# Kernel tuning notes

Hardware: AMD Instinct MI355X
Metric: run time of the kernel (lower is better)

Reference implementation:

```python
import jax, jax.numpy as jnp
import numpy as np

D = 128          # hidden_channels
NU = 50000       # num user nodes
NI = 50000       # num item nodes
E = 600000       # edges per edge type
SLOPE = 0.01     # F.leaky_relu default negative_slope


def setup_inputs() -> dict:
    key = jax.random.key(0)
    ks = jax.random.split(key, 24)
    ws = 1.0 / np.sqrt(D)  # xavier-ish scale

    def W2(i):  # stacked [n_layers=2, D, D] weight
        return jax.random.normal(ks[i], (2, D, D), jnp.float32) * ws

    def B2(i):  # stacked [2, D] bias
        return jax.random.normal(ks[i], (2, D), jnp.float32) * 0.01

    inp = {
        "x_user": jax.random.normal(ks[0], (NU, D), jnp.float32),
        "x_item": jax.random.normal(ks[1], (NI, D), jnp.float32),
        # row 0 = src indices, row 1 = dst indices
        "ei_ui": jax.random.randint(ks[2], (2, E), 0, NU),  # user -> item (dst in [0,NI))
        "ei_iu": jax.random.randint(ks[3], (2, E), 0, NI),  # item -> user (dst in [0,NU))
        # per-node-type q/k/v Linear params, stacked over the 2 layers
        "q_w_user": W2(4),  "q_b_user": B2(5),
        "k_w_user": W2(6),  "k_b_user": B2(7),
        "v_w_user": W2(8),  "v_b_user": B2(9),
        "q_w_item": W2(10), "q_b_item": B2(11),
        "k_w_item": W2(12), "k_b_item": B2(13),
        "v_w_item": W2(14), "v_b_item": B2(15),
        # per-edge-type bilinear W, stacked over the 2 layers
        "W_ui": W2(16),
        "W_iu": W2(17),
    }
    return inp


def _edge_agg(x_src, x_dst, qw, qb, kw, kb, vw, vb, W, src, dst, n_dst):
    # torch Linear: x @ w.T + b
    q = x_src @ qw.T + qb            # [Nsrc, D]
    k = x_dst @ kw.T + kb            # [Ndst, D]
    v = x_src @ vw.T + vb            # [Nsrc, D]
    qW = q @ W                       # project on nodes (cheaper than per-edge)
    # per-edge bilinear score q_src . W . k_dst / sqrt(D)
    score = jnp.sum(qW[src] * k[dst], axis=-1) * (1.0 / np.sqrt(D))  # [E]
    alpha = jax.nn.softmax(jax.nn.leaky_relu(score, SLOPE))          # softmax over edges
    msg = alpha[:, None] * v[src]                                    # [E, D]
    return jax.ops.segment_sum(msg, dst, num_segments=n_dst)


def _layer(x_u, x_i, ei_ui, ei_iu, p, l):
    # edge type (user, rates, item): q/v from src type (user), k from dst type (item)
    agg_i = _edge_agg(x_u, x_i,
                      p["q_w_user"][l], p["q_b_user"][l],
                      p["k_w_item"][l], p["k_b_item"][l],
                      p["v_w_user"][l], p["v_b_user"][l],
                      p["W_ui"][l], ei_ui[0], ei_ui[1], NI)
    # edge type (item, rev_rates, user)
    agg_u = _edge_agg(x_i, x_u,
                      p["q_w_item"][l], p["q_b_item"][l],
                      p["k_w_user"][l], p["k_b_user"][l],
                      p["v_w_item"][l], p["v_b_item"][l],
                      p["W_iu"][l], ei_iu[0], ei_iu[1], NU)
    # out_dict initialized with x_dst.clone(), then scatter_add
    return x_u + agg_u, x_i + agg_i


def reference(x_user, x_item, ei_ui, ei_iu,
              q_w_user, q_b_user, k_w_user, k_b_user, v_w_user, v_b_user,
              q_w_item, q_b_item, k_w_item, k_b_item, v_w_item, v_b_item,
              W_ui, W_iu):
    p = dict(q_w_user=q_w_user, q_b_user=q_b_user, k_w_user=k_w_user,
             k_b_user=k_b_user, v_w_user=v_w_user, v_b_user=v_b_user,
             q_w_item=q_w_item, q_b_item=q_b_item, k_w_item=k_w_item,
             k_b_item=k_b_item, v_w_item=v_w_item, v_b_item=v_b_item,
             W_ui=W_ui, W_iu=W_iu)
    x_u, x_i = _layer(x_user, x_item, ei_ui, ei_iu, p, 0)  # conv1
    x_u, x_i = _layer(x_u, x_i, ei_ui, ei_iu, p, 1)        # conv2
    return jnp.concatenate([x_u, x_i], axis=0)  # [NU+NI, D]
```

## Files before the change

### kernel.cpp

```cpp
#include <hip/hip_runtime.h>
#include <stdint.h>

#define D 128

typedef __attribute__((ext_vector_type(8))) short bf16x8;
typedef __attribute__((ext_vector_type(4))) float f32x4;
typedef __attribute__((ext_vector_type(2))) float f32x2;
typedef unsigned short u16;
typedef unsigned char u8;
typedef unsigned int u32;

static __device__ __forceinline__ float b2f(u16 u) {
  return __uint_as_float(((unsigned)u) << 16);
}
static __device__ __forceinline__ u16 f2b(float f) {
  unsigned u = __float_as_uint(f);
  return (u16)((u + 0x7fffu + ((u >> 16) & 1u)) >> 16);
}

#if defined(__has_builtin)
#if __has_builtin(__builtin_amdgcn_cvt_pk_f32_fp8) && __has_builtin(__builtin_amdgcn_cvt_pk_fp8_f32)
#define HW_FP8 1
#endif
#endif

static __device__ __forceinline__ u8 enc_fp8(float f) {
#ifdef HW_FP8
  int p = __builtin_amdgcn_cvt_pk_fp8_f32(f, 0.f, 0, false);
  return (u8)(p & 0xff);
#else
  float a = fabsf(f);
  unsigned s = (__float_as_uint(f) >> 31) << 7;
  if (a < 7.8125e-3f) {
    int m = (int)(a * 512.f + 0.5f);
    if (m > 7) m = 7;
    return (u8)(s | m);
  }
  int e; float mant = frexpf(a, &e);
  int E = e + 6;
  int m = (int)((2.f * mant - 1.f) * 8.f + 0.5f);
  if (m == 8) { m = 0; E++; }
  if (E > 15 || (E == 15 && m > 6)) { E = 15; m = 6; }
  if (E < 1) return (u8)s;
  return (u8)(s | (E << 3) | m);
#endif
}

static __device__ __forceinline__ float dec1_fp8(u8 b) {
  int e = (b >> 3) & 15, m = b & 7;
  float mag = e ? ldexpf((float)(8 + m), e - 10) : ldexpf((float)m, -9);
  return (b & 128) ? -mag : mag;
}

static __device__ __forceinline__ void dec8_fp8(u32 lo, u32 hi, float* o) {
#ifdef HW_FP8
  f32x2 a = __builtin_amdgcn_cvt_pk_f32_fp8((int)lo, false);
  f32x2 b = __builtin_amdgcn_cvt_pk_f32_fp8((int)lo, true);
  f32x2 c = __builtin_amdgcn_cvt_pk_f32_fp8((int)hi, false);
  f32x2 d = __builtin_amdgcn_cvt_pk_f32_fp8((int)hi, true);
  o[0] = a.x; o[1] = a.y; o[2] = b.x; o[3] = b.y;
  o[4] = c.x; o[5] = c.y; o[6] = d.x; o[7] = d.y;
#else
  u32 w[2] = {lo, hi};
  u8* p = (u8*)w;
#pragma unroll
  for (int i = 0; i < 8; ++i) o[i] = dec1_fp8(p[i]);
#endif
}

template <int CTRL>
static __device__ __forceinline__ float dpp_add_f(float x) {
  int y = __builtin_amdgcn_update_dpp(0, __float_as_int(x), CTRL, 0xf, 0xf, true);
  return x + __int_as_float(y);
}

__global__ void prep_fused(const float* __restrict__ qwu, const float* __restrict__ qbu,
                           const float* __restrict__ qwi, const float* __restrict__ qbi,
                           const float* __restrict__ Wui, const float* __restrict__ Wiu,
                           u16* __restrict__ Mt, float* __restrict__ bq) {
  int c = blockIdx.y, d = blockIdx.x, j = threadIdx.x;
  int l = c & 1, type = c >> 1;
  const float* qw = (type ? qwi : qwu) + l * D * D;
  const float* qb = (type ? qbi : qbu) + l * D;
  const float* W  = (type ? Wiu : Wui) + l * D * D;
  float acc = 0.f;
  for (int cc = 0; cc < D; ++cc) acc += qw[cc * D + d] * W[cc * D + j];
  Mt[((size_t)c * D + j) * D + d] = f2b(acc);
  if (d == 0) {
    float ba = 0.f;
    for (int cc = 0; cc < D; ++cc) ba += qb[cc] * W[cc * D + j];
    bq[c * D + j] = ba;
  }
}

__global__ void cast_w(const float* __restrict__ kwu, const float* __restrict__ kwi,
                       const float* __restrict__ vwu, const float* __restrict__ vwi,
                       u16* __restrict__ Wb) {
  int y = blockIdx.y;
  const float* s = (y == 0) ? kwu : (y == 1) ? kwi : (y == 2) ? vwu : vwi;
  int i = blockIdx.x * 256 + threadIdx.x;
  Wb[(size_t)y * 2 * D * D + i] = f2b(s[i]);
}

__global__ void cast_x(const float* __restrict__ x, u16* __restrict__ xb, int n2) {
  int i = blockIdx.x * 256 + threadIdx.x;
  if (i < n2) {
    float2 v = ((const float2*)x)[i];
    ((unsigned*)xb)[i] = (unsigned)f2b(v.x) | ((unsigned)f2b(v.y) << 16);
  }
}

__global__ void zero_i(int* __restrict__ p, int n) {
  int i = blockIdx.x * 256 + threadIdx.x;
  if (i < n) p[i] = 0;
}

__global__ __launch_bounds__(256) void bhist(const int* __restrict__ dui,
                                             const int* __restrict__ diu,
                                             int* __restrict__ cnt_ui,
                                             int* __restrict__ cnt_iu, int E) {
  __shared__ int h[256];
  int t = threadIdx.x;
  h[t] = 0;
  __syncthreads();
  const int* dp = blockIdx.y ? diu : dui;
  int e0 = blockIdx.x * 1024;
#pragma unroll
  for (int i = 0; i < 4; ++i) {
    int e = e0 + i * 256 + t;
    if (e < E) atomicAdd(&h[dp[e] >> 8], 1);
  }
  __syncthreads();
  int* out = blockIdx.y ? cnt_iu : cnt_ui;
  if (h[t]) atomicAdd(&out[t], h[t]);
}

__global__ __launch_bounds__(256) void bscan(const int* __restrict__ cnt_ui,
                                             const int* __restrict__ cnt_iu,
                                             int* __restrict__ base_ui, int* __restrict__ base_iu,
                                             int* __restrict__ cur_ui, int* __restrict__ cur_iu,
                                             int* __restrict__ rp_ui, int* __restrict__ rp_iu,
                                             int nb_ui, int nb_iu, int n_ui, int n_iu, int E) {
  __shared__ int sh[256];
  int t = threadIdx.x;
  int v = (t < nb_ui) ? cnt_ui[t] : 0;
  sh[t] = v;
  __syncthreads();
  for (int off = 1; off < 256; off <<= 1) {
    int u = (t >= off) ? sh[t - off] : 0;
    __syncthreads();
    sh[t] += u;
    __syncthreads();
  }
  int ex = sh[t] - v;
  if (t < nb_ui) { base_ui[t] = ex; cur_ui[t] = ex; }
  if (t == 0) { base_ui[nb_ui] = E; rp_ui[n_ui] = E; }
  __syncthreads();
  v = (t < nb_iu) ? cnt_iu[t] : 0;
  sh[t] = v;
  __syncthreads();
  for (int off = 1; off < 256; off <<= 1) {
    int u = (t >= off) ? sh[t - off] : 0;
    __syncthreads();
    sh[t] += u;
    __syncthreads();
  }
  ex = sh[t] - v;
  if (t < nb_iu) { base_iu[t] = ex; cur_iu[t] = ex; }
  if (t == 0) { base_iu[nb_iu] = E; rp_iu[n_iu] = E; }
}

__global__ __launch_bounds__(256) void bscatter(
    const int* __restrict__ sui, const int* __restrict__ dui,
    const int* __restrict__ siu, const int* __restrict__ diu,
    int* __restrict__ cur_ui, int* __restrict__ cur_iu,
    u32* __restrict__ bb_ui, u32* __restrict__ bb_iu, int E) {
  __shared__ int h[256], rbase[256], c2[256];
  int t = threadIdx.x;
  const int* sp = blockIdx.y ? siu : sui;
  const int* dp = blockIdx.y ? diu : dui;
  int* gc = blockIdx.y ? cur_iu : cur_ui;
  u32* bb = blockIdx.y ? bb_iu : bb_ui;
  h[t] = 0;
  c2[t] = 0;
  __syncthreads();
  int e0 = blockIdx.x * 1024;
  u32 pr[4];
  int bk[4];
  bool act[4];
#pragma unroll
  for (int i = 0; i < 4; ++i) {
    int e = e0 + i * 256 + t;
    act[i] = e < E;
    if (act[i]) {
      int s = sp[e], d2 = dp[e];
      pr[i] = ((u32)d2 << 16) | (u32)s;
      bk[i] = d2 >> 8;
      atomicAdd(&h[bk[i]], 1);
    }
  }
  __syncthreads();
  if (h[t]) rbase[t] = atomicAdd(&gc[t], h[t]);
  __syncthreads();
#pragma unroll
  for (int i = 0; i < 4; ++i) {
    if (act[i]) {
      int r = atomicAdd(&c2[bk[i]], 1);
      bb[rbase[bk[i]] + r] = pr[i];
    }
  }
}

__global__ __launch_bounds__(256) void bsort(
    const u32* __restrict__ bb_ui, const u32* __restrict__ bb_iu,
    const int* __restrict__ base_ui, const int* __restrict__ base_iu,
    int* __restrict__ rp_ui, int* __restrict__ rp_iu,
    int* __restrict__ cs_ui, int* __restrict__ cs_iu,
    int nb_ui, int n_ui, int n_iu) {
  int b = blockIdx.x;
  const u32* bb; const int* base; int* rp; int* cs; int n;
  if (b < nb_ui) { bb = bb_ui; base = base_ui; rp = rp_ui; cs = cs_ui; n = n_ui; }
  else { b -= nb_ui; bb = bb_iu; base = base_iu; rp = rp_iu; cs = cs_iu; n = n_iu; }
  int lo = base[b], hi = base[b + 1];
  __shared__ int h[256], sh[256], cur[256];
  int t = threadIdx.x;
  h[t] = 0;
  __syncthreads();
  for (int j = lo + t; j < hi; j += 256) atomicAdd(&h[(bb[j] >> 16) & 255], 1);
  __syncthreads();
  int v = h[t];
  sh[t] = v;
  __syncthreads();
  for (int off = 1; off < 256; off <<= 1) {
    int u = (t >= off) ? sh[t - off] : 0;
    __syncthreads();
    sh[t] += u;
    __syncthreads();
  }
  int ex = lo + sh[t] - v;
  int gd = (b << 8) + t;
  if (gd < n) rp[gd] = ex;
  cur[t] = ex;
  __syncthreads();
  for (int j = lo + t; j < hi; j += 256) {
    u32 pr = bb[j];
    int p = atomicAdd(&cur[(pr >> 16) & 255], 1);
    cs[p] = (int)(pr & 0xffffu);
  }
}

__global__ __launch_bounds__(256) void gemm3(
    const u16* __restrict__ xu, const u16* __restrict__ xi,
    const u16* __restrict__ wqu, const u16* __restrict__ wku, const u16* __restrict__ wvu,
    const float* __restrict__ bqu, const float* __restrict__ bku, const float* __restrict__ bvu,
    const u16* __restrict__ wqi, const u16* __restrict__ wki, const u16* __restrict__ wvi,
    const float* __restrict__ bqi, const float* __restrict__ bki, const float* __restrict__ bvi,
    u8* __restrict__ Tqv_u, u16* __restrict__ Tk_u,
    u8* __restrict__ Tqv_i, u16* __restrict__ Tk_i,
    int gu, int nu, int ni) {
  __shared__ __align__(16) u16 wlds[128 * 136];
  int bx = blockIdx.x, y = blockIdx.y;
  bool item = bx >= gu;
  if (item) bx -= gu;
  const u16* x = item ? xi : xu;
  int nrows = item ? ni : nu;
  const u16* wt; const float* bias;
  if (y == 0)      { wt = item ? wqi : wqu; bias = item ? bqi : bqu; }
  else if (y == 1) { wt = item ? wki : wku; bias = item ? bki : bku; }
  else             { wt = item ? wvi : wvu; bias = item ? bvi : bvu; }
  u8* Tqv = item ? Tqv_i : Tqv_u;
  u16* Tk = item ? Tk_i : Tk_u;

  int t = threadIdx.x;
#pragma unroll
  for (int i = 0; i < 8; ++i) {
    int idx = t + 256 * i;
    int n = idx >> 4, kc = idx & 15;
    ((bf16x8*)wlds)[n * 17 + kc] = ((const bf16x8*)wt)[idx];
  }
  __syncthreads();
  int wave = t >> 6, lane = t & 63;
  int m = lane & 15, quad = lane >> 4;
  int row0 = bx * 64 + wave * 16;
  int arow = row0 + m;
  const bf16x8* xv = (const bf16x8*)(x + (size_t)(arow < nrows ? arow : 0) * D);
  f32x4 acc[8];
#pragma unroll
  for (int n = 0; n < 8; ++n) acc[n] = (f32x4){0.f, 0.f, 0.f, 0.f};
#pragma unroll
  for (int kk = 0; kk < 4; ++kk) {
    bf16x8 a = xv[kk * 4 + quad];
#pragma unroll
    for (int n = 0; n < 8; ++n) {
      bf16x8 b = ((const bf16x8*)wlds)[(n * 16 + m) * 17 + kk * 4 + quad];
      acc[n] = __builtin_amdgcn_mfma_f32_16x16x32_bf16(a, b, acc[n], 0, 0, 0);
    }
  }
  if (y == 1) {
#pragma unroll
    for (int n = 0; n < 8; ++n) {
      float bb = bias[n * 16 + m];
#pragma unroll
      for (int r = 0; r < 4; ++r) {
        int orow = row0 + quad * 4 + r;
        if (orow < nrows) Tk[(size_t)orow * D + n * 16 + m] = f2b(acc[n][r] + bb);
      }
    }
  } else {
    int vo = (y == 0) ? 0 : 8;
#pragma unroll
    for (int n = 0; n < 8; ++n) {
      float bb = bias[n * 16 + m];
      int dim = n * 16 + m;
      int boff = ((dim >> 3) << 4) + (dim & 7) + vo;
#pragma unroll
      for (int r = 0; r < 4; ++r) {
        int orow = row0 + quad * 4 + r;
        if (orow < nrows) Tqv[(size_t)orow * 256 + boff] = enc_fp8(acc[n][r] + bb);
      }
    }
  }
}

static __device__ __forceinline__ void do_edge(uint4 w, bool act, const float* kx,
                                               float* acc, float& z) {
  float qx[8], vx[8];
  dec8_fp8(w.x, w.y, qx);
  dec8_fp8(w.z, w.w, vx);
  float dot = 0.f;
#pragma unroll
  for (int i = 0; i < 8; ++i) dot = fmaf(qx[i], kx[i], dot);
  dot = dpp_add_f<0xB1>(dot);
  dot = dpp_add_f<0x4E>(dot);
  dot = dpp_add_f<0x128>(dot);
  dot = dpp_add_f<0x124>(dot);
  float sc = dot * 0.08838834764831845f;
  sc = (sc > 0.f) ? sc : 0.01f * sc;
  float p = act ? __expf(sc) : 0.f;
  z += p;
#pragma unroll
  for (int i = 0; i < 8; ++i) acc[i] = fmaf(p, vx[i], acc[i]);
}

__global__ __launch_bounds__(256, 8) void agg_pass(
    const u8* __restrict__ Tqv_u, const u16* __restrict__ Tk_u,
    const u8* __restrict__ Tqv_i, const u16* __restrict__ Tk_i,
    const int* __restrict__ rp_ui, const int* __restrict__ cs_ui,
    const int* __restrict__ rp_iu, const int* __restrict__ cs_iu,
    float* __restrict__ agg_u, float* __restrict__ agg_i,
    float* __restrict__ zpart, int gai, int ni, int nu) {
  int bx = blockIdx.x;
  const u8* Pqv; const u16* Pk; const int* rp; const int* cs;
  float* agg; float* zp; int ndst;
  if (bx < gai) { Pqv = Tqv_u; Pk = Tk_i; rp = rp_ui; cs = cs_ui; agg = agg_i; zp = zpart; ndst = ni; }
  else { bx -= gai; Pqv = Tqv_i; Pk = Tk_u; rp = rp_iu; cs = cs_iu; agg = agg_u; zp = zpart + 1024; ndst = nu; }
  int wave = threadIdx.x >> 6, lane = threadIdx.x & 63;
  int d = bx * 4 + wave;
  int sub = lane & 15;
  int quad = lane >> 4;
  float z = 0.f;
  float acc[8] = {0.f, 0.f, 0.f, 0.f, 0.f, 0.f, 0.f, 0.f};
  if (d < ndst) {
    bf16x8 kf = *(const bf16x8*)(Pk + (size_t)d * D + sub * 8);
    int beg = rp[d], end = rp[d + 1];
    float kx[8];
#pragma unroll
    for (int i = 0; i < 8; ++i) kx[i] = b2f((u16)((short*)&kf)[i]);
    const u8* Pq = Pqv + sub * 16;
    int iters = (end - beg + 7) >> 3;
    for (int it = 0; it < iters; ++it) {
      int j0 = beg + it * 8 + quad;
      int j1 = j0 + 4;
      bool a0 = j0 < end, a1 = j1 < end;
      int s0 = a0 ? cs[j0] : 0;
      int s1 = a1 ? cs[j1] : 0;
      uint4 w0 = *(const uint4*)(Pq + (size_t)s0 * 256);
      uint4 w1 = *(const uint4*)(Pq + (size_t)s1 * 256);
      do_edge(w0, a0, kx, acc, z);
      do_edge(w1, a1, kx, acc, z);
    }
#pragma unroll
    for (int i = 0; i < 8; ++i) {
      acc[i] += __shfl_xor(acc[i], 16, 64);
      acc[i] += __shfl_xor(acc[i], 32, 64);
    }
    if (quad == 0) {
      float* ap = agg + (size_t)d * D + sub * 8;
      ((f32x4*)ap)[0] = (f32x4){acc[0], acc[1], acc[2], acc[3]};
      ((f32x4*)ap)[1] = (f32x4){acc[4], acc[5], acc[6], acc[7]};
    }
    z += __shfl_xor(z, 16, 64);
    z += __shfl_xor(z, 32, 64);
  }
  __shared__ float ps[4];
  if (lane == 0) ps[wave] = z;
  __syncthreads();
  if (threadIdx.x == 0)
    unsafeAtomicAdd(&zp[blockIdx.x & 1023], ps[0] + ps[1] + ps[2] + ps[3]);
}

__global__ void zreduce(const float* __restrict__ zpart, float* __restrict__ zinv) {
  const float* zp = zpart + blockIdx.x * 1024;
  int t = threadIdx.x;
  float s = 0.f;
  for (int i = t; i < 1024; i += 256) s += zp[i];
  __shared__ float red[256];
  red[t] = s;
  __syncthreads();
  for (int k = 128; k > 0; k >>= 1) {
    if (t < k) red[t] += red[t + k];
    __syncthreads();
  }
  if (t == 0) zinv[blockIdx.x] = 1.0f / red[0];
}

__global__ void update_x(const float* __restrict__ xu, const float* __restrict__ xi,
                         const float* __restrict__ aggu, const float* __restrict__ aggi,
                         const float* __restrict__ zinv,
                         float* __restrict__ ou, float* __restrict__ oi,
                         u16* __restrict__ bu, u16* __restrict__ bi,
                         int nu, int ni, int wb) {
  int i = blockIdx.x * 256 + threadIdx.x;
  float zu = zinv[1];
  float zi = zinv[0];
  if (i < nu) {
    float v = xu[i] + aggu[i] * zu;
    ou[i] = v;
    if (wb) bu[i] = f2b(v);
  } else if (i < nu + ni) {
    int j = i - nu;
    float v = xi[j] + aggi[j] * zi;
    oi[j] = v;
    if (wb) bi[j] = f2b(v);
  }
}

extern "C" void kernel_launch(void* const* d_in, const int* in_sizes, int n_in,
                              void* d_out, int out_size, void* d_ws, size_t ws_size,
                              hipStream_t stream) {
  const float* xu_in = (const float*)d_in[0];
  const float* xi_in = (const float*)d_in[1];
  const int* ei_ui = (const int*)d_in[2];
  const int* ei_iu = (const int*)d_in[3];
  const float* qwu = (const float*)d_in[4];
  const float* qbu = (const float*)d_in[5];
  const float* kwu = (const float*)d_in[6];
  const float* kbu = (const float*)d_in[7];
  const float* vwu = (const float*)d_in[8];
  const float* vbu = (const float*)d_in[9];
  const float* qwi = (const float*)d_in[10];
  const float* qbi = (const float*)d_in[11];
  const float* kwi = (const float*)d_in[12];
  const float* kbi = (const float*)d_in[13];
  const float* vwi = (const float*)d_in[14];
  const float* vbi = (const float*)d_in[15];
  const float* Wui = (const float*)d_in[16];
  const float* Wiu = (const float*)d_in[17];

  int NU = in_sizes[0] / D;
  int NI = in_sizes[1] / D;
  int E  = in_sizes[2] / 2;

  char* w = (char*)d_ws;
  float* agg_u = (float*)w;  w += (size_t)NU * D * 4;
  float* agg_i = (float*)w;  w += (size_t)NI * D * 4;
  int* bcnt_ui = (int*)w;    w += 256 * 4;
  int* bcnt_iu = (int*)w;    w += 256 * 4;
  float* zpart = (float*)w;  w += 4096 * 4;
  float* zinv  = (float*)w;  w += 64;
  float* bq    = (float*)w;  w += 4 * D * 4;
  int* base_ui = (int*)w;    w += 260 * 4;
  int* base_iu = (int*)w;    w += 260 * 4;
  int* cur_ui  = (int*)w;    w += 256 * 4;
  int* cur_iu  = (int*)w;    w += 256 * 4;
  int* rp_ui = (int*)w;      w += (size_t)(NI + 4) * 4;
  int* rp_iu = (int*)w;      w += (size_t)(NU + 4) * 4;
  int* cs_ui = (int*)w;      w += (size_t)E * 4;
  int* cs_iu = (int*)w;      w += (size_t)E * 4;
  u32* bb_ui = (u32*)w;      w += (size_t)E * 4;
  u32* bb_iu = (u32*)w;      w += (size_t)E * 4;
  u16* Mt  = (u16*)w;        w += (size_t)4 * D * D * 2;
  u16* Wb  = (u16*)w;        w += (size_t)8 * D * D * 2;
  u16* xub = (u16*)w;        w += (size_t)NU * D * 2;
  u16* xib = (u16*)w;        w += (size_t)NI * D * 2;
  u16* Tk_u = (u16*)w;       w += (size_t)NU * D * 2;
  u16* Tk_i = (u16*)w;       w += (size_t)NI * D * 2;
  u8* Tqv_u = (u8*)w;        w += (size_t)NU * 256;
  u8* Tqv_i = (u8*)w;

  float* out_u = (float*)d_out;
  float* out_i = out_u + (size_t)NU * D;

  prep_fused<<<dim3(128, 4), 128, 0, stream>>>(qwu, qbu, qwi, qbi, Wui, Wiu, Mt, bq);
  cast_w<<<dim3(128, 4), 256, 0, stream>>>(kwu, kwi, vwu, vwi, Wb);
  cast_x<<<(NU * D / 2 + 255) / 256, 256, 0, stream>>>(xu_in, xub, NU * D / 2);
  cast_x<<<(NI * D / 2 + 255) / 256, 256, 0, stream>>>(xi_in, xib, NI * D / 2);

  int nb_ui = (NI + 255) >> 8;
  int nb_iu = (NU + 255) >> 8;
  zero_i<<<18, 256, 0, stream>>>(bcnt_ui, 512 + 4096);
  int geb = (E + 1023) / 1024;
  bhist<<<dim3(geb, 2), 256, 0, stream>>>(ei_ui + E, ei_iu + E, bcnt_ui, bcnt_iu, E);
  bscan<<<1, 256, 0, stream>>>(bcnt_ui, bcnt_iu, base_ui, base_iu, cur_ui, cur_iu,
                               rp_ui, rp_iu, nb_ui, nb_iu, NI, NU, E);
  bscatter<<<dim3(geb, 2), 256, 0, stream>>>(ei_ui, ei_ui + E, ei_iu, ei_iu + E,
                                             cur_ui, cur_iu, bb_ui, bb_iu, E);
  bsort<<<nb_ui + nb_iu, 256, 0, stream>>>(bb_ui, bb_iu, base_ui, base_iu,
                                           rp_ui, rp_iu, cs_ui, cs_iu, nb_ui, NI, NU);

  int gu = (NU + 63) / 64, gi = (NI + 63) / 64;
  int gau = (NU + 3) / 4, gai = (NI + 3) / 4;
  int gup = (NU * D + NI * D + 255) / 256;

  for (int l = 0; l < 2; ++l) {
    gemm3<<<dim3(gu + gi, 3), 256, 0, stream>>>(
        xub, xib,
        Mt + (size_t)l * D * D, Wb + (size_t)(0 + l) * D * D, Wb + (size_t)(4 + l) * D * D,
        bq + l * D, kbu + l * D, vbu + l * D,
        Mt + (size_t)(2 + l) * D * D, Wb + (size_t)(2 + l) * D * D, Wb + (size_t)(6 + l) * D * D,
        bq + (2 + l) * D, kbi + l * D, vbi + l * D,
        Tqv_u, Tk_u, Tqv_i, Tk_i, gu, NU, NI);
    agg_pass<<<gai + gau, 256, 0, stream>>>(
        Tqv_u, Tk_u, Tqv_i, Tk_i, rp_ui, cs_ui, rp_iu, cs_iu,
        agg_u, agg_i, zpart + (size_t)l * 2 * 1024, gai, NI, NU);
    zreduce<<<2, 256, 0, stream>>>(zpart + (size_t)l * 2 * 1024, zinv + l * 2);
    if (l == 0)
      update_x<<<gup, 256, 0, stream>>>(xu_in, xi_in, agg_u, agg_i, zinv + l * 2,
                                        out_u, out_i, xub, xib, NU * D, NI * D, 1);
    else
      update_x<<<gup, 256, 0, stream>>>(out_u, out_i, agg_u, agg_i, zinv + l * 2,
                                        out_u, out_i, nullptr, nullptr, NU * D, NI * D, 0);
  }
}
```

Baseline: 497.5 us.

## Map one destination node per 16-lane group and fold score scale into K

The aggregation kernel now gives each 16-lane group its own destination node (16 nodes per block) instead of spreading one node's edges across a whole wave. This removes the cross-quad shuffle reductions and keeps short edge lists from leaving lanes idle, at the cost of divergence when degrees differ within a wave. The 1/sqrt(D) scale and log2(e) are folded into K at GEMM time so the per-edge exp becomes exp2 with no extra multiply. This is valid because leaky_relu commutes with positive scaling. Aggregate stores are also made nontemporal.

```diff
diff --git a/kernel.cpp b/kernel.cpp
--- a/kernel.cpp
+++ b/kernel.cpp
@@ -9,6 +9,8 @@
 typedef unsigned short u16;
 typedef unsigned char u8;
 typedef unsigned int u32;
+
+#define KSCALE (0.08838834764831845f * 1.4426950408889634f)
 
 static __device__ __forceinline__ float b2f(u16 u) {
   return __uint_as_float(((unsigned)u) << 16);
@@ -303,7 +305,7 @@
 #pragma unroll
       for (int r = 0; r < 4; ++r) {
         int orow = row0 + quad * 4 + r;
-        if (orow < nrows) Tk[(size_t)orow * D + n * 16 + m] = f2b(acc[n][r] + bb);
+        if (orow < nrows) Tk[(size_t)orow * D + n * 16 + m] = f2b((acc[n][r] + bb) * KSCALE);
       }
     }
   } else {
@@ -334,9 +336,8 @@
   dot = dpp_add_f<0x4E>(dot);
   dot = dpp_add_f<0x128>(dot);
   dot = dpp_add_f<0x124>(dot);
-  float sc = dot * 0.08838834764831845f;
-  sc = (sc > 0.f) ? sc : 0.01f * sc;
-  float p = act ? __expf(sc) : 0.f;
+  float sc = (dot > 0.f) ? dot : 0.01f * dot;
+  float p = act ? exp2f(sc) : 0.f;
   z += p;
 #pragma unroll
   for (int i = 0; i < 8; ++i) acc[i] = fmaf(p, vx[i], acc[i]);
@@ -355,43 +356,40 @@
   if (bx < gai) { Pqv = Tqv_u; Pk = Tk_i; rp = rp_ui; cs = cs_ui; agg = agg_i; zp = zpart; ndst = ni; }
   else { bx -= gai; Pqv = Tqv_i; Pk = Tk_u; rp = rp_iu; cs = cs_iu; agg = agg_u; zp = zpart + 1024; ndst = nu; }
   int wave = threadIdx.x >> 6, lane = threadIdx.x & 63;
-  int d = bx * 4 + wave;
+  int grp = lane >> 4;
   int sub = lane & 15;
-  int quad = lane >> 4;
+  int d = bx * 16 + wave * 4 + grp;
+  bool active = d < ndst;
+  int dd = active ? d : 0;
   float z = 0.f;
   float acc[8] = {0.f, 0.f, 0.f, 0.f, 0.f, 0.f, 0.f, 0.f};
-  if (d < ndst) {
-    bf16x8 kf = *(const bf16x8*)(Pk + (size_t)d * D + sub * 8);
-    int beg = rp[d], end = rp[d + 1];
-    float kx[8];
-#pragma unroll
-    for (int i = 0; i < 8; ++i) kx[i] = b2f((u16)((short*)&kf)[i]);
-    const u8* Pq = Pqv + sub * 16;
-    int iters = (end - beg + 7) >> 3;
-    for (int it = 0; it < iters; ++it) {
-      int j0 = beg + it * 8 + quad;
-      int j1 = j0 + 4;
-      bool a0 = j0 < end, a1 = j1 < end;
-      int s0 = a0 ? cs[j0] : 0;
-      int s1 = a1 ? cs[j1] : 0;
-      uint4 w0 = *(const uint4*)(Pq + (size_t)s0 * 256);
-      uint4 w1 = *(const uint4*)(Pq + (size_t)s1 * 256);
-      do_edge(w0, a0, kx, acc, z);
-      do_edge(w1, a1, kx, acc, z);
-    }
-#pragma unroll
-    for (int i = 0; i < 8; ++i) {
-      acc[i] += __shfl_xor(acc[i], 16, 64);
-      acc[i] += __shfl_xor(acc[i], 32, 64);
-    }
-    if (quad == 0) {
-      float* ap = agg + (size_t)d * D + sub * 8;
-      ((f32x4*)ap)[0] = (f32x4){acc[0], acc[1], acc[2], acc[3]};
-      ((f32x4*)ap)[1] = (f32x4){acc[4], acc[5], acc[6], acc[7]};
-    }
-    z += __shfl_xor(z, 16, 64);
-    z += __shfl_xor(z, 32, 64);
-  }
+
+  bf16x8 kf = *(const bf16x8*)(Pk + (size_t)dd * D + sub * 8);
+  float kx[8];
+#pragma unroll
+  for (int i = 0; i < 8; ++i) kx[i] = b2f((u16)((short*)&kf)[i]);
+
+  int beg = rp[dd];
+  int end = active ? rp[dd + 1] : beg;
+  const u8* Pq = Pqv + sub * 16;
+  for (int j = beg; j < end; j += 2) {
+    int s0 = cs[j];
+    int j1 = j + 1;
+    bool a1 = j1 < end;
+    int s1 = a1 ? cs[j1] : s0;
+    uint4 w0 = *(const uint4*)(Pq + (size_t)s0 * 256);
+    uint4 w1 = *(const uint4*)(Pq + (size_t)s1 * 256);
+    do_edge(w0, true, kx, acc, z);
+    do_edge(w1, a1, kx, acc, z);
+  }
+
+  if (active) {
+    float* ap = agg + (size_t)d * D + sub * 8;
+    __builtin_nontemporal_store((f32x4){acc[0], acc[1], acc[2], acc[3]}, (f32x4*)ap);
+    __builtin_nontemporal_store((f32x4){acc[4], acc[5], acc[6], acc[7]}, (f32x4*)ap + 1);
+  }
+  z += __shfl_xor(z, 16, 64);
+  z += __shfl_xor(z, 32, 64);
   __shared__ float ps[4];
   if (lane == 0) ps[wave] = z;
   __syncthreads();
@@ -509,7 +507,7 @@
                                            rp_ui, rp_iu, cs_ui, cs_iu, nb_ui, NI, NU);
 
   int gu = (NU + 63) / 64, gi = (NI + 63) / 64;
-  int gau = (NU + 3) / 4, gai = (NI + 3) / 4;
+  int gau = (NU + 15) / 16, gai = (NI + 15) / 16;
   int gup = (NU * D + NI * D + 255) / 256;
 
   for (int l = 0; l < 2; ++l) {
```

Result: slower. 565.6 us (+13.7%).
